# Performance work log

Measured on AMD Instinct MI355X. Metric: run time of the kernel, lower is better.

The kernel has to match this reference:

```python
import jax, jax.numpy as jnp
import numpy as np
from jax import lax

B, L = 4, 1024
D_MODEL, D_STATE, D_CONV = 512, 16, 4
D_INNER = 2 * D_MODEL          # expand=2
DT_RANK = D_MODEL // 16        # ceil(512/16)=32
K_EXPERTS = 2                  # num_experts_per_token; only first k experts are used
EPS = 1e-5


def setup_inputs() -> dict:
    key = jax.random.key(0)
    ks = jax.random.split(key, 14)
    def n(k, shape, scale=0.02):
        return jax.random.normal(k, shape, jnp.float32) * scale
    # Mamba S4D-real init for A: A_log = log(1..d_state) broadcast over channels
    A_log = jnp.log(jnp.broadcast_to(jnp.arange(1, D_STATE + 1, dtype=jnp.float32), (D_INNER, D_STATE)))
    return {
        "x": jax.random.normal(ks[0], (B, L, D_MODEL), jnp.float32),
        "in_proj_w": n(ks[1], (2 * D_INNER, D_MODEL)),
        "conv_w": n(ks[2], (D_INNER, 1, D_CONV), 0.1),
        "conv_b": n(ks[3], (D_INNER,), 0.1),
        "x_proj_w": n(ks[4], (DT_RANK + 2 * D_STATE, D_INNER)),
        "dt_proj_w": n(ks[5], (D_INNER, DT_RANK), 0.1),
        "dt_proj_b": n(ks[6], (D_INNER,), 0.1),
        "A_log": A_log,
        "D_skip": jnp.ones((D_INNER,), jnp.float32),
        "out_proj_w": n(ks[7], (D_MODEL, D_INNER)),
        "moe_w1": n(ks[8], (K_EXPERTS, 2 * D_MODEL, D_MODEL)),
        "moe_b1": n(ks[9], (K_EXPERTS, 2 * D_MODEL)),
        "moe_w2": n(ks[10], (K_EXPERTS, D_MODEL, 2 * D_MODEL)),
        "moe_b2": n(ks[11], (K_EXPERTS, D_MODEL)),
    }


def _layernorm(x):
    # fresh nn.LayerNorm each forward: weight=1, bias=0, eps=1e-5
    mu = jnp.mean(x, -1, keepdims=True)
    var = jnp.mean(jnp.square(x - mu), -1, keepdims=True)
    return (x - mu) / jnp.sqrt(var + EPS)


def _mamba(x, in_proj_w, conv_w, conv_b, x_proj_w, dt_proj_w, dt_proj_b, A_log, D_skip, out_proj_w):
    b = x.shape[0]
    xz = x @ in_proj_w.T                               # (b, L, 2*d_inner)
    xc, z = jnp.split(xz, 2, axis=-1)
    # causal depthwise conv1d (torch pads both sides with d_conv-1 then slices [:L])
    conv = lax.conv_general_dilated(
        xc.transpose(0, 2, 1), conv_w, (1,), [(D_CONV - 1, 0)],
        feature_group_count=D_INNER) + conv_b[None, :, None]
    xs = jax.nn.silu(conv).transpose(0, 2, 1)          # (b, L, d_inner)
    dbc = xs @ x_proj_w.T                              # (b, L, dt_rank + 2*d_state)
    dt = dbc[..., :DT_RANK]
    Bm = dbc[..., DT_RANK:DT_RANK + D_STATE]           # (b, L, d_state)
    Cm = dbc[..., DT_RANK + D_STATE:]                  # (b, L, d_state)
    delta = jax.nn.softplus(dt @ dt_proj_w.T + dt_proj_b)  # (b, L, d_inner)
    A = -jnp.exp(A_log)                                # (d_inner, d_state)
    dA = jnp.exp(jnp.einsum('bld,dn->bldn', delta, A))     # (b, L, d_inner, d_state)
    dBx = (delta * xs)[..., None] * Bm[:, :, None, :]       # (b, L, d_inner, d_state)

    def step(h, inp):
        dA_t, dBx_t, C_t = inp
        h = dA_t * h + dBx_t                           # (b, d_inner, d_state)
        y = jnp.einsum('bdn,bn->bd', h, C_t)
        return h, y

    h0 = jnp.zeros((b, D_INNER, D_STATE), x.dtype)
    _, ys = lax.scan(step, h0, (dA.transpose(1, 0, 2, 3), dBx.transpose(1, 0, 2, 3), Cm.transpose(1, 0, 2)))
    y = ys.transpose(1, 0, 2) + xs * D_skip            # (b, L, d_inner)
    y = y * jax.nn.silu(z)
    return y @ out_proj_w.T                            # (b, L, d_model)


def reference(x, in_proj_w, conv_w, conv_b, x_proj_w, dt_proj_w, dt_proj_b,
              A_log, D_skip, out_proj_w, moe_w1, moe_b1, moe_w2, moe_b2):
    skip = x
    h = _layernorm(x)
    h = _mamba(h, in_proj_w, conv_w, conv_b, x_proj_w, dt_proj_w, dt_proj_b, A_log, D_skip, out_proj_w) + h
    h = _layernorm(h)
    # static 'MoE': unweighted average of the first K_EXPERTS dense FFNs
    a = jax.nn.relu(jnp.einsum('bld,ekd->belk', h, moe_w1) + moe_b1[None, :, None, :])
    moe = jnp.einsum('belk,edk->beld', a, moe_w2) + moe_b2[None, :, None, :]
    return jnp.mean(moe, axis=1) + skip
```

## Files before the change

### kernel.cpp

```cpp
#include <hip/hip_runtime.h>
#include <hip/hip_bf16.h>

#define BB 4
#define LL 1024
#define DM 512
#define DI 1024
#define DS 16
#define DTR 32
#define MM (BB*LL)

#define ACT_NONE 0
#define ACT_RELU 1
#define ACT_SP   2

#define CHUNK 32
#define NCH (LL/CHUNK)
#define NSTATE 65536

typedef __attribute__((ext_vector_type(8))) __bf16 bf16x8;
typedef __attribute__((ext_vector_type(8))) unsigned short us8;
typedef __attribute__((ext_vector_type(4))) float f32x4;

__device__ __forceinline__ unsigned short f2bf(float f) {
  union { float f; unsigned int u; } a; a.f = f;
  unsigned int r = a.u + 0x7fffu + ((a.u >> 16) & 1u);
  return (unsigned short)(r >> 16);
}
__device__ __forceinline__ float b2f(unsigned short u) {
  union { unsigned int i; float f; } a; a.i = (unsigned int)u << 16; return a.f;
}

__device__ __forceinline__ bf16x8 ld_frag(const unsigned short* p) {
  us8 s = *(const us8*)p;
  return __builtin_bit_cast(bf16x8, s);
}

__device__ __forceinline__ void gload16(const void* g, void* l) {
  __builtin_amdgcn_global_load_lds(
      (const __attribute__((address_space(1))) void*)g,
      (__attribute__((address_space(3))) void*)l, 16, 0, 0);
}

__global__ __launch_bounds__(256) void prep_ln_kernel(
    const float* __restrict__ x,
    const float* __restrict__ in_proj_w, const float* __restrict__ x_proj_w,
    const float* __restrict__ dt_proj_w, const float* __restrict__ out_proj_w,
    const float* __restrict__ moe_w1,    const float* __restrict__ moe_w2,
    const float* __restrict__ moe_b2,
    float* __restrict__ h1, unsigned short* __restrict__ h1b,
    unsigned short* __restrict__ inpb,  unsigned short* __restrict__ xpjb,
    unsigned short* __restrict__ dtpb,  unsigned short* __restrict__ outpb,
    unsigned short* __restrict__ w1b,   unsigned short* __restrict__ w2cb,
    float* __restrict__ b2avg)
{
  __shared__ float red[8];
  int bid = blockIdx.x;
  if (bid < MM) {
    int row = bid;
    const float* p = x + (size_t)row * DM;
    float2 v = ((const float2*)p)[threadIdx.x];
    float s  = v.x + v.y;
    float ss = v.x*v.x + v.y*v.y;
    for (int o = 32; o; o >>= 1) { s += __shfl_down(s, o); ss += __shfl_down(ss, o); }
    int wid = threadIdx.x >> 6, lane = threadIdx.x & 63;
    if (lane == 0) { red[wid] = s; red[4+wid] = ss; }
    __syncthreads();
    s  = red[0]+red[1]+red[2]+red[3];
    ss = red[4]+red[5]+red[6]+red[7];
    float mu = s * (1.f/DM);
    float var = ss * (1.f/DM) - mu*mu;
    float rstd = rsqrtf(var + 1e-5f);
    float2 o2; o2.x = (v.x-mu)*rstd; o2.y = (v.y-mu)*rstd;
    ((float2*)(h1 + (size_t)row*DM))[threadIdx.x] = o2;
    ushort2 u; u.x = f2bf(o2.x); u.y = f2bf(o2.y);
    ((ushort2*)(h1b + (size_t)row*DM))[threadIdx.x] = u;
    return;
  }
  int i = (bid - MM) * 256 + threadIdx.x;
  int i4 = i * 4;
  auto cvt4 = [&](const float* src, unsigned short* dst) {
    float4 v = ((const float4*)src)[i];
    ushort4 o; o.x = f2bf(v.x); o.y = f2bf(v.y); o.z = f2bf(v.z); o.w = f2bf(v.w);
    ((ushort4*)dst)[i] = o;
  };
  if (i4 < 2*DI*DM) cvt4(in_proj_w, inpb);
  if (i4 < 64*DI)   cvt4(x_proj_w, xpjb);
  if (i4 < DI*DTR)  cvt4(dt_proj_w, dtpb);
  if (i4 < DM*DI)   cvt4(out_proj_w, outpb);
  if (i4 < 2*(2*DM)*DM) cvt4(moe_w1, w1b);
  if (i4 < DM*2*DI) {
    #pragma unroll
    for (int j = 0; j < 4; ++j) {
      int idx = i4 + j;
      int nrow = idx >> 11;
      int t = idx & (2*DI - 1);
      int e = t >> 10;
      int k = t & (DI - 1);
      w2cb[idx] = f2bf(moe_w2[((size_t)e*DM + nrow)*DI + k]);
    }
  }
  if (i4 < DM) {
    #pragma unroll
    for (int j = 0; j < 4; ++j)
      b2avg[i4+j] = 0.5f * (moe_b2[i4+j] + moe_b2[DM + i4+j]);
  }
}

__global__ __launch_bounds__(256) void ln_kernel(const float* __restrict__ in,
                                                 float* __restrict__ outf,
                                                 unsigned short* __restrict__ outb) {
  int row = blockIdx.x;
  const float* p = in + (size_t)row * DM;
  float2 v = ((const float2*)p)[threadIdx.x];
  float s  = v.x + v.y;
  float ss = v.x*v.x + v.y*v.y;
  for (int o = 32; o; o >>= 1) { s += __shfl_down(s, o); ss += __shfl_down(ss, o); }
  __shared__ float red[8];
  int wid = threadIdx.x >> 6, lane = threadIdx.x & 63;
  if (lane == 0) { red[wid] = s; red[4+wid] = ss; }
  __syncthreads();
  s  = red[0]+red[1]+red[2]+red[3];
  ss = red[4]+red[5]+red[6]+red[7];
  float mu = s * (1.f/DM);
  float var = ss * (1.f/DM) - mu*mu;
  float rstd = rsqrtf(var + 1e-5f);
  float2 o2; o2.x = (v.x-mu)*rstd; o2.y = (v.y-mu)*rstd;
  if (outf) ((float2*)(outf + (size_t)row*DM))[threadIdx.x] = o2;
  if (outb) {
    ushort2 u; u.x = f2bf(o2.x); u.y = f2bf(o2.y);
    ((ushort2*)(outb + (size_t)row*DM))[threadIdx.x] = u;
  }
}

template<int BM, int BN, int BK, int WR, int WC, int FM, int FN, int ACT,
         bool OUTF, bool OUTB>
__global__ __launch_bounds__(256) void gemm_mfma(
    const unsigned short* __restrict__ A, int lda,
    const unsigned short* __restrict__ B, int ldb,
    const float* __restrict__ bias,
    const float* __restrict__ res, int ldres,
    float* __restrict__ Cf, unsigned short* __restrict__ Cb, int ldc,
    int K, float scale, int nbx)
{
  static_assert(WR*WC == 4 && WR*FM*16 == BM && WC*FN*16 == BN, "geom");
  constexpr int ATILE = BM*BK, BTILE = BN*BK;
  constexpr int AL = ATILE/2048, BL = BTILE/2048;
  constexpr bool SWZ = (BK >= 64);
  constexpr int SH = (BK == 64) ? 7 : 8;
  __shared__ unsigned short As[2*ATILE];
  __shared__ unsigned short Bs[2*BTILE];
  const int tid = threadIdx.x;
  const int nwg = gridDim.x;
  const int bid = blockIdx.x;
  const int cpx = nwg >> 3;
  const int wid = ((nwg & 7) == 0) ? ((bid & 7)*cpx + (bid >> 3)) : bid;
  const int bm = (wid / nbx) * BM;
  const int bn = (wid % nbx) * BN;
  const int w = tid >> 6, lane = tid & 63;
  const int wr = w / WC, wc = w % WC;
  const int rl = lane & 15, kg = lane >> 4;

  auto stage = [&](int buf, int k0) {
    #pragma unroll
    for (int it = 0; it < AL; ++it) {
      int o = (it*256 + tid) * 16;
      int os = SWZ ? (o ^ (((o>>SH)&7)<<4)) : o;
      int e = os >> 1;
      int r = e / BK, c = e % BK;
      gload16(A + (size_t)(bm + r)*lda + k0 + c, (char*)As + buf*ATILE*2 + o);
    }
    #pragma unroll
    for (int it = 0; it < BL; ++it) {
      int o = (it*256 + tid) * 16;
      int os = SWZ ? (o ^ (((o>>SH)&7)<<4)) : o;
      int e = os >> 1;
      int r = e / BK, c = e % BK;
      gload16(B + (size_t)(bn + r)*ldb + k0 + c, (char*)Bs + buf*BTILE*2 + o);
    }
  };

  f32x4 acc[FM][FN];
  #pragma unroll
  for (int m = 0; m < FM; ++m)
    #pragma unroll
    for (int n = 0; n < FN; ++n) { f32x4 z = {0.f,0.f,0.f,0.f}; acc[m][n] = z; }

  auto compute = [&](int buf) {
    #pragma unroll
    for (int kk = 0; kk < BK/32; ++kk) {
      bf16x8 af[FM], bfv[FN];
      #pragma unroll
      for (int m = 0; m < FM; ++m) {
        int byte = ((wr*FM*16 + m*16 + rl)*BK + kk*32 + kg*8) * 2;
        if (SWZ) byte ^= ((byte>>SH)&7)<<4;
        af[m] = ld_frag((const unsigned short*)((const char*)As + buf*ATILE*2 + byte));
      }
      #pragma unroll
      for (int n = 0; n < FN; ++n) {
        int byte = ((wc*FN*16 + n*16 + rl)*BK + kk*32 + kg*8) * 2;
        if (SWZ) byte ^= ((byte>>SH)&7)<<4;
        bfv[n] = ld_frag((const unsigned short*)((const char*)Bs + buf*BTILE*2 + byte));
      }
      #pragma unroll
      for (int m = 0; m < FM; ++m)
        #pragma unroll
        for (int n = 0; n < FN; ++n)
          acc[m][n] = __builtin_amdgcn_mfma_f32_16x16x32_bf16(bfv[n], af[m], acc[m][n], 0, 0, 0);
    }
  };

  stage(0, 0);
  const int nk = K / BK;
  for (int it = 0; it < nk; ++it) {
    if (it + 1 < nk) {
      stage((it&1)^1, (it+1)*BK);
      asm volatile("s_waitcnt vmcnt(%0)" :: "i"(AL+BL) : "memory");
    } else {
      asm volatile("s_waitcnt vmcnt(0)" ::: "memory");
    }
    __builtin_amdgcn_s_barrier();
    compute(it & 1);
    __builtin_amdgcn_s_barrier();
  }

  #pragma unroll
  for (int m = 0; m < FM; ++m) {
    int row = bm + wr*FM*16 + m*16 + rl;
    #pragma unroll
    for (int n = 0; n < FN; ++n) {
      int colb = bn + wc*FN*16 + n*16 + kg*4;
      float4 bv = {0.f,0.f,0.f,0.f};
      if (bias) bv = *(const float4*)(bias + colb);
      float vv[4];
      #pragma unroll
      for (int j = 0; j < 4; ++j) {
        float v = acc[m][n][j] * scale + (&bv.x)[j];
        if (ACT == ACT_RELU) v = fmaxf(v, 0.f);
        if (ACT == ACT_SP)   v = fmaxf(v, 0.f) + log1pf(__expf(-fabsf(v)));
        vv[j] = v;
      }
      if (res) {
        float4 r = *(const float4*)(res + (size_t)row*ldres + colb);
        vv[0] += r.x; vv[1] += r.y; vv[2] += r.z; vv[3] += r.w;
      }
      size_t off = (size_t)row*ldc + colb;
      if (OUTF) {
        float4 o; o.x = vv[0]; o.y = vv[1]; o.z = vv[2]; o.w = vv[3];
        *(float4*)(Cf + off) = o;
      }
      if (OUTB) {
        ushort4 o; o.x = f2bf(vv[0]); o.y = f2bf(vv[1]);
        o.z = f2bf(vv[2]); o.w = f2bf(vv[3]);
        *(ushort4*)(Cb + off) = o;
      }
    }
  }
}

__global__ __launch_bounds__(256) void conv_silu_kernel(
    const unsigned short* __restrict__ xzb, const float* __restrict__ conv_w,
    const float* __restrict__ conv_b, unsigned short* __restrict__ xsb)
{
  int t = blockIdx.x * 256 + threadIdx.x;
  int d8 = (t & (DI/8 - 1)) * 8;
  int l = (t >> 7) & (LL-1);
  int b = t >> 17;
  size_t base = (size_t)(b*LL) * 2*DI + d8;
  float acc[8];
  #pragma unroll
  for (int j = 0; j < 8; ++j) acc[j] = conv_b[d8+j];
  #pragma unroll
  for (int k = 0; k < 4; ++k) {
    int ll = l - 3 + k;
    if (ll >= 0) {
      us8 v = *(const us8*)(xzb + base + (size_t)ll * 2*DI);
      #pragma unroll
      for (int j = 0; j < 8; ++j)
        acc[j] = fmaf(conv_w[(d8+j)*4 + k], b2f((unsigned short)v[j]), acc[j]);
    }
  }
  us8 o;
  #pragma unroll
  for (int j = 0; j < 8; ++j) {
    float s = acc[j];
    float v = s / (1.f + __expf(-s));
    o[j] = (unsigned short)f2bf(v);
  }
  *(us8*)(xsb + (size_t)((b*LL + l)*DI) + d8) = o;
}

__global__ __launch_bounds__(256) void scan_A(
    const unsigned short* __restrict__ deltab,
    const unsigned short* __restrict__ xsb,
    const float* __restrict__ dbc,
    const float* __restrict__ A_log,
    float* __restrict__ S, float* __restrict__ Qb)
{
  int blk = blockIdx.x;
  int dq = blk & 3;
  int c  = (blk >> 2) & (NCH-1);
  int b  = blk >> 7;
  int tid = threadIdx.x;
  int d = dq*256 + tid;
  float An[16];
  #pragma unroll
  for (int n = 0; n < 16; n += 4) {
    float4 a = *(const float4*)(A_log + d*DS + n);
    An[n+0] = -__expf(a.x) * 1.44269504f;
    An[n+1] = -__expf(a.y) * 1.44269504f;
    An[n+2] = -__expf(a.z) * 1.44269504f;
    An[n+3] = -__expf(a.w) * 1.44269504f;
  }
  __shared__ float s_B[CHUNK][16];
  for (int i = tid; i < CHUNK*16; i += 256) {
    int l = i >> 4, n = i & 15;
    s_B[l][n] = dbc[((size_t)(b*LL) + c*CHUNK + l)*64 + 32 + n];
  }
  __syncthreads();
  float h[16];
  #pragma unroll
  for (int n = 0; n < 16; ++n) h[n] = 0.f;
  float Ssum = 0.f;
  size_t rowbase = ((size_t)(b*LL) + c*CHUNK)*DI + d;
  #pragma unroll 4
  for (int l = 0; l < CHUNK; ++l) {
    float delta = b2f(deltab[rowbase + (size_t)l*DI]);
    float xv    = b2f(xsb   [rowbase + (size_t)l*DI]);
    float dx = delta * xv;
    Ssum += delta;
    #pragma unroll
    for (int n = 0; n < 16; ++n)
      h[n] = fmaf(exp2f(delta*An[n]), h[n], dx * s_B[l][n]);
  }
  S[c*(BB*DI) + b*DI + d] = Ssum;
  float* q = Qb + (size_t)c*NSTATE + (size_t)(b*DI + d)*16;
  #pragma unroll
  for (int n = 0; n < 16; n += 4) {
    float4 v; v.x = h[n]; v.y = h[n+1]; v.z = h[n+2]; v.w = h[n+3];
    *(float4*)(q + n) = v;
  }
}

__global__ __launch_bounds__(256) void scan_stitch(
    const float* __restrict__ S, const float* __restrict__ Qb,
    const float* __restrict__ A_log, float* __restrict__ H)
{
  int t = blockIdx.x * 256 + threadIdx.x;
  int bd = t >> 4, n = t & 15;
  int d = bd & (DI-1);
  float An = -__expf(A_log[d*DS + n]) * 1.44269504f;
  float h = 0.f;
  for (int c = 0; c < NCH; ++c) {
    H[(size_t)c*NSTATE + t] = h;
    h = fmaf(exp2f(S[c*(BB*DI) + bd]*An), h, Qb[(size_t)c*NSTATE + t]);
  }
}

__global__ __launch_bounds__(256) void scan_B(
    const unsigned short* __restrict__ deltab,
    const unsigned short* __restrict__ xsb,
    const unsigned short* __restrict__ xzb,
    const float* __restrict__ dbc,
    const float* __restrict__ A_log,
    const float* __restrict__ D_skip,
    const float* __restrict__ H,
    unsigned short* __restrict__ ymulb)
{
  int blk = blockIdx.x;
  int dq = blk & 3;
  int c  = (blk >> 2) & (NCH-1);
  int b  = blk >> 7;
  int tid = threadIdx.x;
  int d = dq*256 + tid;
  float An[16];
  #pragma unroll
  for (int n = 0; n < 16; n += 4) {
    float4 a = *(const float4*)(A_log + d*DS + n);
    An[n+0] = -__expf(a.x) * 1.44269504f;
    An[n+1] = -__expf(a.y) * 1.44269504f;
    An[n+2] = -__expf(a.z) * 1.44269504f;
    An[n+3] = -__expf(a.w) * 1.44269504f;
  }
  float Dd = D_skip[d];
  __shared__ float s_B[CHUNK][16], s_C[CHUNK][16];
  for (int i = tid; i < CHUNK*16; i += 256) {
    int l = i >> 4, n = i & 15;
    size_t row = (size_t)(b*LL) + c*CHUNK + l;
    s_B[l][n] = dbc[row*64 + 32 + n];
    s_C[l][n] = dbc[row*64 + 48 + n];
  }
  __syncthreads();
  float h[16];
  const float* hp = H + (size_t)c*NSTATE + (size_t)(b*DI + d)*16;
  #pragma unroll
  for (int n = 0; n < 16; n += 4) {
    float4 v = *(const float4*)(hp + n);
    h[n] = v.x; h[n+1] = v.y; h[n+2] = v.z; h[n+3] = v.w;
  }
  size_t rowbase = ((size_t)(b*LL) + c*CHUNK)*DI + d;
  size_t zbase   = ((size_t)(b*LL) + c*CHUNK)*2*DI + DI + d;
  #pragma unroll 4
  for (int l = 0; l < CHUNK; ++l) {
    float delta = b2f(deltab[rowbase + (size_t)l*DI]);
    float xv    = b2f(xsb   [rowbase + (size_t)l*DI]);
    float zv    = b2f(xzb   [zbase   + (size_t)l*2*DI]);
    float dx = delta * xv;
    float y = 0.f;
    #pragma unroll
    for (int n = 0; n < 16; ++n) {
      h[n] = fmaf(exp2f(delta*An[n]), h[n], dx * s_B[l][n]);
      y = fmaf(h[n], s_C[l][n], y);
    }
    float sz = zv / (1.f + __expf(-zv));
    float v = (y + xv*Dd) * sz;
    ymulb[rowbase + (size_t)l*DI] = f2bf(v);
  }
}

extern "C" void kernel_launch(void* const* d_in, const int* in_sizes, int n_in,
                              void* d_out, int out_size, void* d_ws, size_t ws_size,
                              hipStream_t stream) {
  const float* x         = (const float*)d_in[0];
  const float* in_proj_w = (const float*)d_in[1];
  const float* conv_w    = (const float*)d_in[2];
  const float* conv_b    = (const float*)d_in[3];
  const float* x_proj_w  = (const float*)d_in[4];
  const float* dt_proj_w = (const float*)d_in[5];
  const float* dt_proj_b = (const float*)d_in[6];
  const float* A_log     = (const float*)d_in[7];
  const float* D_skip    = (const float*)d_in[8];
  const float* out_proj_w= (const float*)d_in[9];
  const float* moe_w1    = (const float*)d_in[10];
  const float* moe_b1    = (const float*)d_in[11];
  const float* moe_w2    = (const float*)d_in[12];
  const float* moe_b2    = (const float*)d_in[13];
  float* out = (float*)d_out;

  float* p = (float*)d_ws;
  float* h1    = p; p += 2097152;
  float* h2    = p; p += 2097152;
  float* dbc   = p; p += 262144;
  float* Sbuf  = p; p += 131072;
  float* Qbuf  = p; p += 2097152;
  float* Hbuf  = p; p += 2097152;
  float* b2avg = p; p += 1024;
  unsigned short* h1b    = (unsigned short*)p; p += 1048576;
  unsigned short* xzb    = (unsigned short*)p; p += 4194304;
  unsigned short* xsb    = (unsigned short*)p; p += 2097152;
  unsigned short* deltab = (unsigned short*)p; p += 2097152;
  unsigned short* dbcb   = (unsigned short*)p; p += 131072;
  unsigned short* ymulb  = (unsigned short*)p; p += 2097152;
  unsigned short* h2lnb  = (unsigned short*)p; p += 1048576;
  unsigned short* acatb  = (unsigned short*)p; p += 4194304;
  unsigned short* inpb   = (unsigned short*)p; p += 524288;
  unsigned short* xpjb   = (unsigned short*)p; p += 32768;
  unsigned short* dtpb   = (unsigned short*)p; p += 16384;
  unsigned short* outpb  = (unsigned short*)p; p += 262144;
  unsigned short* w1b    = (unsigned short*)p; p += 524288;
  unsigned short* w2cb   = (unsigned short*)p; p += 524288;

  prep_ln_kernel<<<MM + 1024, 256, 0, stream>>>(x, in_proj_w, x_proj_w, dt_proj_w,
                                                out_proj_w, moe_w1, moe_w2, moe_b2,
                                                h1, h1b, inpb, xpjb, dtpb, outpb,
                                                w1b, w2cb, b2avg);
  gemm_mfma<128,128,64,2,2,4,4,ACT_NONE,false,true><<<512, 256, 0, stream>>>(
      h1b, DM, inpb, DM, nullptr, nullptr, 0, nullptr, xzb, 2*DI, DM, 1.f, 16);
  conv_silu_kernel<<<(MM*DI/8)/256, 256, 0, stream>>>(xzb, conv_w, conv_b, xsb);
  gemm_mfma<64,64,128,2,2,2,2,ACT_NONE,true,true><<<64, 256, 0, stream>>>(
      xsb, DI, xpjb, DI, nullptr, nullptr, 0, dbc, dbcb, 64, DI, 1.f, 1);
  gemm_mfma<128,128,32,2,2,4,4,ACT_SP,false,true><<<256, 256, 0, stream>>>(
      dbcb, 64, dtpb, DTR, dt_proj_b, nullptr, 0, nullptr, deltab, DI, DTR, 1.f, 8);
  scan_A<<<BB*NCH*4, 256, 0, stream>>>(deltab, xsb, dbc, A_log, Sbuf, Qbuf);
  scan_stitch<<<NSTATE/256, 256, 0, stream>>>(Sbuf, Qbuf, A_log, Hbuf);
  scan_B<<<BB*NCH*4, 256, 0, stream>>>(deltab, xsb, xzb, dbc, A_log, D_skip, Hbuf, ymulb);
  gemm_mfma<64,64,128,2,2,2,2,ACT_NONE,true,false><<<512, 256, 0, stream>>>(
      ymulb, DI, outpb, DI, nullptr, h1, DM, h2, nullptr, DM, DI, 1.f, 8);
  ln_kernel<<<MM, 256, 0, stream>>>(h2, nullptr, h2lnb);
  gemm_mfma<128,128,64,2,2,4,4,ACT_RELU,false,true><<<512, 256, 0, stream>>>(
      h2lnb, DM, w1b, DM, moe_b1, nullptr, 0, nullptr, acatb, 2*DI, DM, 1.f, 16);
  gemm_mfma<64,64,128,2,2,2,2,ACT_NONE,true,false><<<512, 256, 0, stream>>>(
      acatb, 2*DI, w2cb, 2*DI, b2avg, x, DM, out, nullptr, DM, 2*DI, 0.5f, 8);
}
```

Baseline: 210.8 us.

## Store residual activations in bf16, enlarge scan chunk, retile output GEMMs

The fp32 h1 and h2 residual buffers are dropped. h1 is now read from its bf16 copy as the residual in the out_proj GEMM, which writes h2 in bf16 for the second layernorm, cutting intermediate memory traffic. The scan chunk size goes from 32 to 64, halving the number of chunks and the size of the stitch state buffers. The out_proj and MoE down-projection GEMMs switch from 64x64 to 128x64 tiles on half as many blocks. Rounding the residual and the layernorm input to bf16 adds numerical error. The longer chunks also lengthen each block's serial scan.

```diff
diff --git a/kernel.cpp b/kernel.cpp
--- a/kernel.cpp
+++ b/kernel.cpp
@@ -13,7 +13,7 @@
 #define ACT_RELU 1
 #define ACT_SP   2
 
-#define CHUNK 32
+#define CHUNK 64
 #define NCH (LL/CHUNK)
 #define NSTATE 65536
 
@@ -47,7 +47,7 @@
     const float* __restrict__ dt_proj_w, const float* __restrict__ out_proj_w,
     const float* __restrict__ moe_w1,    const float* __restrict__ moe_w2,
     const float* __restrict__ moe_b2,
-    float* __restrict__ h1, unsigned short* __restrict__ h1b,
+    unsigned short* __restrict__ h1b,
     unsigned short* __restrict__ inpb,  unsigned short* __restrict__ xpjb,
     unsigned short* __restrict__ dtpb,  unsigned short* __restrict__ outpb,
     unsigned short* __restrict__ w1b,   unsigned short* __restrict__ w2cb,
@@ -70,9 +70,7 @@
     float mu = s * (1.f/DM);
     float var = ss * (1.f/DM) - mu*mu;
     float rstd = rsqrtf(var + 1e-5f);
-    float2 o2; o2.x = (v.x-mu)*rstd; o2.y = (v.y-mu)*rstd;
-    ((float2*)(h1 + (size_t)row*DM))[threadIdx.x] = o2;
-    ushort2 u; u.x = f2bf(o2.x); u.y = f2bf(o2.y);
+    ushort2 u; u.x = f2bf((v.x-mu)*rstd); u.y = f2bf((v.y-mu)*rstd);
     ((ushort2*)(h1b + (size_t)row*DM))[threadIdx.x] = u;
     return;
   }
@@ -106,14 +104,13 @@
   }
 }
 
-__global__ __launch_bounds__(256) void ln_kernel(const float* __restrict__ in,
-                                                 float* __restrict__ outf,
+__global__ __launch_bounds__(256) void ln_kernel(const unsigned short* __restrict__ in,
                                                  unsigned short* __restrict__ outb) {
   int row = blockIdx.x;
-  const float* p = in + (size_t)row * DM;
-  float2 v = ((const float2*)p)[threadIdx.x];
-  float s  = v.x + v.y;
-  float ss = v.x*v.x + v.y*v.y;
+  ushort2 uv = ((const ushort2*)(in + (size_t)row*DM))[threadIdx.x];
+  float vx = b2f(uv.x), vy = b2f(uv.y);
+  float s  = vx + vy;
+  float ss = vx*vx + vy*vy;
   for (int o = 32; o; o >>= 1) { s += __shfl_down(s, o); ss += __shfl_down(ss, o); }
   __shared__ float red[8];
   int wid = threadIdx.x >> 6, lane = threadIdx.x & 63;
@@ -124,21 +121,17 @@
   float mu = s * (1.f/DM);
   float var = ss * (1.f/DM) - mu*mu;
   float rstd = rsqrtf(var + 1e-5f);
-  float2 o2; o2.x = (v.x-mu)*rstd; o2.y = (v.y-mu)*rstd;
-  if (outf) ((float2*)(outf + (size_t)row*DM))[threadIdx.x] = o2;
-  if (outb) {
-    ushort2 u; u.x = f2bf(o2.x); u.y = f2bf(o2.y);
-    ((ushort2*)(outb + (size_t)row*DM))[threadIdx.x] = u;
-  }
+  ushort2 u; u.x = f2bf((vx-mu)*rstd); u.y = f2bf((vy-mu)*rstd);
+  ((ushort2*)(outb + (size_t)row*DM))[threadIdx.x] = u;
 }
 
 template<int BM, int BN, int BK, int WR, int WC, int FM, int FN, int ACT,
-         bool OUTF, bool OUTB>
+         bool OUTF, bool OUTB, bool RESB>
 __global__ __launch_bounds__(256) void gemm_mfma(
     const unsigned short* __restrict__ A, int lda,
     const unsigned short* __restrict__ B, int ldb,
     const float* __restrict__ bias,
-    const float* __restrict__ res, int ldres,
+    const void* __restrict__ res, int ldres,
     float* __restrict__ Cf, unsigned short* __restrict__ Cb, int ldc,
     int K, float scale, int nbx)
 {
@@ -240,8 +233,13 @@
         vv[j] = v;
       }
       if (res) {
-        float4 r = *(const float4*)(res + (size_t)row*ldres + colb);
-        vv[0] += r.x; vv[1] += r.y; vv[2] += r.z; vv[3] += r.w;
+        if (RESB) {
+          ushort4 r = *(const ushort4*)((const unsigned short*)res + (size_t)row*ldres + colb);
+          vv[0] += b2f(r.x); vv[1] += b2f(r.y); vv[2] += b2f(r.z); vv[3] += b2f(r.w);
+        } else {
+          float4 r = *(const float4*)((const float*)res + (size_t)row*ldres + colb);
+          vv[0] += r.x; vv[1] += r.y; vv[2] += r.z; vv[3] += r.w;
+        }
       }
       size_t off = (size_t)row*ldc + colb;
       if (OUTF) {
@@ -299,7 +297,7 @@
   int blk = blockIdx.x;
   int dq = blk & 3;
   int c  = (blk >> 2) & (NCH-1);
-  int b  = blk >> 7;
+  int b  = blk >> 6;
   int tid = threadIdx.x;
   int d = dq*256 + tid;
   float An[16];
@@ -369,7 +367,7 @@
   int blk = blockIdx.x;
   int dq = blk & 3;
   int c  = (blk >> 2) & (NCH-1);
-  int b  = blk >> 7;
+  int b  = blk >> 6;
   int tid = threadIdx.x;
   int d = dq*256 + tid;
   float An[16];
@@ -437,12 +435,10 @@
   float* out = (float*)d_out;
 
   float* p = (float*)d_ws;
-  float* h1    = p; p += 2097152;
-  float* h2    = p; p += 2097152;
   float* dbc   = p; p += 262144;
-  float* Sbuf  = p; p += 131072;
-  float* Qbuf  = p; p += 2097152;
-  float* Hbuf  = p; p += 2097152;
+  float* Sbuf  = p; p += 65536;
+  float* Qbuf  = p; p += 1048576;
+  float* Hbuf  = p; p += 1048576;
   float* b2avg = p; p += 1024;
   unsigned short* h1b    = (unsigned short*)p; p += 1048576;
   unsigned short* xzb    = (unsigned short*)p; p += 4194304;
@@ -450,6 +446,7 @@
   unsigned short* deltab = (unsigned short*)p; p += 2097152;
   unsigned short* dbcb   = (unsigned short*)p; p += 131072;
   unsigned short* ymulb  = (unsigned short*)p; p += 2097152;
+  unsigned short* h2b    = (unsigned short*)p; p += 1048576;
   unsigned short* h2lnb  = (unsigned short*)p; p += 1048576;
   unsigned short* acatb  = (unsigned short*)p; p += 4194304;
   unsigned short* inpb   = (unsigned short*)p; p += 524288;
@@ -461,23 +458,23 @@
 
   prep_ln_kernel<<<MM + 1024, 256, 0, stream>>>(x, in_proj_w, x_proj_w, dt_proj_w,
                                                 out_proj_w, moe_w1, moe_w2, moe_b2,
-                                                h1, h1b, inpb, xpjb, dtpb, outpb,
+                                                h1b, inpb, xpjb, dtpb, outpb,
                                                 w1b, w2cb, b2avg);
-  gemm_mfma<128,128,64,2,2,4,4,ACT_NONE,false,true><<<512, 256, 0, stream>>>(
+  gemm_mfma<128,128,64,2,2,4,4,ACT_NONE,false,true,false><<<512, 256, 0, stream>>>(
       h1b, DM, inpb, DM, nullptr, nullptr, 0, nullptr, xzb, 2*DI, DM, 1.f, 16);
   conv_silu_kernel<<<(MM*DI/8)/256, 256, 0, stream>>>(xzb, conv_w, conv_b, xsb);
-  gemm_mfma<64,64,128,2,2,2,2,ACT_NONE,true,true><<<64, 256, 0, stream>>>(
+  gemm_mfma<64,64,128,2,2,2,2,ACT_NONE,true,true,false><<<64, 256, 0, stream>>>(
       xsb, DI, xpjb, DI, nullptr, nullptr, 0, dbc, dbcb, 64, DI, 1.f, 1);
-  gemm_mfma<128,128,32,2,2,4,4,ACT_SP,false,true><<<256, 256, 0, stream>>>(
+  gemm_mfma<128,128,32,2,2,4,4,ACT_SP,false,true,false><<<256, 256, 0, stream>>>(
       dbcb, 64, dtpb, DTR, dt_proj_b, nullptr, 0, nullptr, deltab, DI, DTR, 1.f, 8);
   scan_A<<<BB*NCH*4, 256, 0, stream>>>(deltab, xsb, dbc, A_log, Sbuf, Qbuf);
   scan_stitch<<<NSTATE/256, 256, 0, stream>>>(Sbuf, Qbuf, A_log, Hbuf);
   scan_B<<<BB*NCH*4, 256, 0, stream>>>(deltab, xsb, xzb, dbc, A_log, D_skip, Hbuf, ymulb);
-  gemm_mfma<64,64,128,2,2,2,2,ACT_NONE,true,false><<<512, 256, 0, stream>>>(
-      ymulb, DI, outpb, DI, nullptr, h1, DM, h2, nullptr, DM, DI, 1.f, 8);
-  ln_kernel<<<MM, 256, 0, stream>>>(h2, nullptr, h2lnb);
-  gemm_mfma<128,128,64,2,2,4,4,ACT_RELU,false,true><<<512, 256, 0, stream>>>(
+  gemm_mfma<128,64,128,2,2,4,2,ACT_NONE,false,true,true><<<256, 256, 0, stream>>>(
+      ymulb, DI, outpb, DI, nullptr, h1b, DM, nullptr, h2b, DM, DI, 1.f, 8);
+  ln_kernel<<<MM, 256, 0, stream>>>(h2b, h2lnb);
+  gemm_mfma<128,128,64,2,2,4,4,ACT_RELU,false,true,false><<<512, 256, 0, stream>>>(
       h2lnb, DM, w1b, DM, moe_b1, nullptr, 0, nullptr, acatb, 2*DI, DM, 1.f, 16);
-  gemm_mfma<64,64,128,2,2,2,2,ACT_NONE,true,false><<<512, 256, 0, stream>>>(
+  gemm_mfma<128,64,128,2,2,4,2,ACT_NONE,true,false,false><<<256, 256, 0, stream>>>(
       acatb, 2*DI, w2cb, 2*DI, b2avg, x, DM, out, nullptr, DM, 2*DI, 0.5f, 8);
 }
```

Result: slower. 239.2 us (+13.4%).
